# Kernel tuning notes

Measured on AMD Instinct MI355X. Metric: run time of the kernel, lower is better.

The kernel has to match this reference:

```python
import jax, jax.numpy as jnp
import numpy as np

BETA = 0.4
EPS = 0.05
NUM_CLASSES = 5


def _model_single(xi, W1, b1, W2, b2):
    # xi: [C, L] single sample -> logits [num_classes]
    h = jnp.tanh(xi.reshape(-1) @ W1 + b1)
    return h @ W2 + b2


def setup_inputs() -> dict:
    key = jax.random.key(0)
    k1, k2, k3, k4 = jax.random.split(key, 4)
    B, C, L, H = 8192, 1, 2048, 1024
    x = jax.random.normal(k1, (B, C, L), dtype=jnp.float32)
    y = jax.random.randint(k2, (B,), 0, NUM_CLASSES)
    W1 = jax.random.normal(k3, (C * L, H), dtype=jnp.float32) * (1.0 / np.sqrt(C * L).astype(np.float32))
    b1 = jnp.zeros((H,), dtype=jnp.float32)
    W2 = jax.random.normal(k4, (H, NUM_CLASSES), dtype=jnp.float32) * (1.0 / np.sqrt(H).astype(np.float32))
    b2 = jnp.zeros((NUM_CLASSES,), dtype=jnp.float32)
    return {"x": x, "y": y, "W1": W1, "b1": b1, "W2": W2, "b2": b2}


def reference(x, y, W1, b1, W2, b2):
    B = x.shape[0]
    # batched model forward (same math the torch loop calls per-sample)
    logits = jnp.tanh(x.reshape(B, -1) @ W1 + b1) @ W2 + b2  # [B, num_classes]

    y_onehot = jax.nn.one_hot(y, NUM_CLASSES, dtype=logits.dtype)
    mse_loss = jnp.mean((logits - y_onehot) ** 2)

    idx = jnp.arange(B)
    z_y = logits[idx, y]  # [B]
    margins = jnp.maximum(1.0 - z_y[:, None] + logits, 0.0)
    margins = margins.at[idx, y].set(0.0)
    margin_loss = margins.sum() / B

    # per-sample L1 norm of d z_y / d x_i: one batched vmap(grad) instead of a python loop
    def z_of_x(xi, yi):
        return _model_single(xi, W1, b1, W2, b2)[yi]

    grads = jax.vmap(jax.grad(z_of_x), in_axes=(0, 0))(x, y)  # [B, C, L]
    w_l1 = jnp.sum(jnp.abs(grads), axis=(1, 2))  # [B]

    R = w_l1 * EPS / (jnp.abs(z_y) + 1e-8)
    nsr_loss = BETA * jnp.mean(jnp.log1p(R))

    correct_mask = jnp.mean((jnp.argmax(logits, axis=1) == y).astype(logits.dtype))
    total_loss = mse_loss + (margin_loss + nsr_loss) * correct_mask
    return total_loss
```

## Files before the change

kernel.cpp:

```cpp
#include <hip/hip_runtime.h>
#include <hip/hip_bf16.h>

typedef unsigned short ushort_t;
typedef unsigned char uchar_t;
typedef __attribute__((ext_vector_type(8))) short short8;
typedef __attribute__((ext_vector_type(8))) unsigned short u16x8;
typedef __attribute__((ext_vector_type(4))) float f32x4;
typedef __attribute__((ext_vector_type(4))) int i32x4;

#define BETA 0.4f
#define EPS_C 0.05f
#define NB 8192
#define NH 1024
#define NL 2048
#define NC 5
#define VS_I8 800.0f
#define WS_I8 1200.0f

static __device__ __forceinline__ float b2f(unsigned short u) {
    union { unsigned int i; float f; } x; x.i = ((unsigned int)u) << 16; return x.f;
}
static __device__ __forceinline__ unsigned short f2b(float f) {
    union { float f; unsigned int i; } x; x.f = f;
    unsigned int i = x.i;
    unsigned int r = (i + 0x7FFFu + ((i >> 16) & 1u)) >> 16;
    return (unsigned short)r;
}
static __device__ __forceinline__ char f2i8(float f, float s) {
    float q = rintf(f * s);
    q = fminf(127.f, fmaxf(-127.f, q));
    return (char)(int)q;
}

static __device__ __forceinline__ void gload16(const ushort_t* g, ushort_t* l) {
    __builtin_amdgcn_global_load_lds((const __attribute__((address_space(1))) void*)g,
                                     (__attribute__((address_space(3))) void*)l, 16, 0, 0);
}
static __device__ __forceinline__ void gload16b(const uchar_t* g, uchar_t* l) {
    __builtin_amdgcn_global_load_lds((const __attribute__((address_space(1))) void*)g,
                                     (__attribute__((address_space(3))) void*)l, 16, 0, 0);
}

#define CFENCE() asm volatile("" ::: "memory")
#define MFMA16(d, a, b) __builtin_amdgcn_mfma_f32_16x16x32_bf16(a, b, d, 0, 0, 0)
#define MFMAI8(d, a, b) __builtin_amdgcn_mfma_i32_16x16x64_i8(a, b, d, 0, 0, 0)

__global__ __launch_bounds__(256) void cvt_kernel(const float* __restrict__ in,
                                                  ushort_t* __restrict__ out, long n) {
    long i = ((long)blockIdx.x * 256 + threadIdx.x) * 8;
    if (i >= n) return;
    const float4 a = *(const float4*)(in + i);
    const float4 b = *(const float4*)(in + i + 4);
    u16x8 o;
    o[0] = f2b(a.x); o[1] = f2b(a.y); o[2] = f2b(a.z); o[3] = f2b(a.w);
    o[4] = f2b(b.x); o[5] = f2b(b.y); o[6] = f2b(b.z); o[7] = f2b(b.w);
    *(u16x8*)(out + i) = o;
}

__global__ __launch_bounds__(256) void trans_kernel(const float* __restrict__ W1,
                                                    ushort_t* __restrict__ W1Tb,
                                                    char* __restrict__ W1i8) {
    __shared__ float tile[32][33];
    const int tx = threadIdx.x & 31, ty = threadIdx.x >> 5;
    const int k0 = blockIdx.x * 32, n0 = blockIdx.y * 32;
#pragma unroll
    for (int i = 0; i < 4; ++i) {
        const float v = W1[(size_t)(k0 + ty + i * 8) * NH + n0 + tx];
        tile[ty + i * 8][tx] = v;
        W1i8[(size_t)(k0 + ty + i * 8) * NH + n0 + tx] = f2i8(v, WS_I8);
    }
    __syncthreads();
#pragma unroll
    for (int i = 0; i < 4; ++i)
        W1Tb[(size_t)(n0 + ty + i * 8) * NL + k0 + tx] = f2b(tile[tx][ty + i * 8]);
}

__global__ __launch_bounds__(256, 2) void g128_1(const ushort_t* __restrict__ A,
                                                 const ushort_t* __restrict__ Bt,
                                                 const float* __restrict__ b1,
                                                 ushort_t* __restrict__ hout) {
    constexpr int K  = 2048;
    constexpr int NT = K / 64;

    __shared__ ushort_t As[2][8192];
    __shared__ ushort_t Bs[2][8192];

    const int tid = threadIdx.x;
    const int wv = tid >> 6, lane = tid & 63;
    const int wm = (wv >> 1) & 1, wn = wv & 1;
    const int fr = lane & 15, fg = lane >> 4;

    const int xcd = blockIdx.x & 7, loc = blockIdx.x >> 3;
    const int bm0 = (xcd * 8 + (loc >> 3)) * 128;
    const int bn0 = (loc & 7) * 128;

    const int srow = lane >> 3;
    const int scol = ((lane & 7) ^ srow) << 3;

#define STA(BUF, KT) {                                                      \
    _Pragma("unroll") for (int c_ = 0; c_ < 4; ++c_) {                      \
        const int row_ = c_ * 32 + wv * 8 + srow;                           \
        gload16(A + (size_t)(bm0 + row_) * K + (KT) * 64 + scol,            \
                &As[BUF][c_ * 2048 + wv * 512]);                            \
    } }
#define STB(BUF, KT) {                                                      \
    _Pragma("unroll") for (int c_ = 0; c_ < 4; ++c_) {                      \
        const int row_ = c_ * 32 + wv * 8 + srow;                           \
        gload16(Bt + (size_t)(bn0 + row_) * K + (KT) * 64 + scol,           \
                &Bs[BUF][c_ * 2048 + wv * 512]);                            \
    } }

    auto ldA = [&](int buf, int mf, int ks) -> short8 {
        const int row = wm * 64 + mf * 16 + fr;
        const int slot = ((ks << 2) + fg) ^ (row & 7);
        return *(const short8*)&As[buf][row * 64 + slot * 8];
    };
    auto ldB = [&](int buf, int nf, int ks) -> short8 {
        const int row = wn * 64 + nf * 16 + fr;
        const int slot = ((ks << 2) + fg) ^ (row & 7);
        return *(const short8*)&Bs[buf][row * 64 + slot * 8];
    };

    f32x4 acc[4][4] = {};

    STA(0, 0) STB(0, 0)
    asm volatile("s_waitcnt vmcnt(0)" ::: "memory");
    CFENCE(); __builtin_amdgcn_s_barrier(); CFENCE();

#define TILE(BUF, TT) {                                                     \
    const int t_ = (TT);                                                    \
    short8 af[4][2], bf[4][2];                                              \
    _Pragma("unroll") for (int n_ = 0; n_ < 4; ++n_) {                      \
        bf[n_][0] = ldB(BUF, n_, 0); bf[n_][1] = ldB(BUF, n_, 1);           \
    }                                                                       \
    _Pragma("unroll") for (int m_ = 0; m_ < 4; ++m_) {                      \
        af[m_][0] = ldA(BUF, m_, 0); af[m_][1] = ldA(BUF, m_, 1);           \
    }                                                                       \
    if (t_ + 1 < NT) { STA(BUF ^ 1, t_ + 1) STB(BUF ^ 1, t_ + 1) }          \
    CFENCE(); __builtin_amdgcn_s_barrier(); CFENCE();                       \
    __builtin_amdgcn_s_setprio(1);                                          \
    _Pragma("unroll") for (int m_ = 0; m_ < 4; ++m_)                        \
        _Pragma("unroll") for (int n_ = 0; n_ < 4; ++n_) {                  \
            acc[m_][n_] = MFMA16(acc[m_][n_], af[m_][0], bf[n_][0]);        \
            acc[m_][n_] = MFMA16(acc[m_][n_], af[m_][1], bf[n_][1]);        \
        }                                                                   \
    __builtin_amdgcn_s_setprio(0);                                          \
    asm volatile("s_waitcnt vmcnt(0)" ::: "memory");                        \
    CFENCE(); __builtin_amdgcn_s_barrier(); CFENCE();                       \
    }

#pragma unroll 1
    for (int t = 0; t < NT; t += 2) {
        TILE(0, t)
        TILE(1, t + 1)
    }
#undef TILE
#undef STA
#undef STB

#pragma unroll
    for (int m = 0; m < 4; ++m)
#pragma unroll
        for (int n = 0; n < 4; ++n) {
            const int col = bn0 + wn * 64 + n * 16 + fr;
            const float bb = b1[col];
            const size_t rbase = (size_t)(bm0 + wm * 64 + m * 16 + fg * 4) * NH + col;
#pragma unroll
            for (int r = 0; r < 4; ++r)
                hout[rbase + (size_t)r * NH] = f2b(tanhf(acc[m][n][r] + bb));
        }
}

__global__ __launch_bounds__(256, 4) void g2i8(const char* __restrict__ A,
                                               const char* __restrict__ Bt,
                                               float* __restrict__ partout) {
    constexpr int K  = 1024;
    constexpr int NT = K / 64;

    __shared__ uchar_t As[2][8192];
    __shared__ uchar_t Bs[2][8192];

    const int tid = threadIdx.x;
    const int wv = tid >> 6, lane = tid & 63;
    const int wm = (wv >> 1) & 1, wn = wv & 1;
    const int fr = lane & 15, fg = lane >> 4;

    const int xcd = blockIdx.x & 7, loc = blockIdx.x >> 3;
    const int bm0 = (xcd * 8 + (loc >> 4)) * 128;
    const int bnIdx = loc & 15;
    const int bn0 = bnIdx * 128;

    const int t8 = tid >> 3, t7 = tid & 7;

#define STAF(BUF, KT) {                                                     \
    _Pragma("unroll") for (int j_ = 0; j_ < 2; ++j_) {                      \
        const int r1_ = j_ * 32 + t8;                                       \
        const int sl_ = (t7 * 2) ^ ((r1_ & 7) << 1);                        \
        const int row_ = 2 * r1_ + (sl_ >> 3);                              \
        const int cb_ = (KT) * 64 + (sl_ & 7) * 8;                          \
        gload16b((const uchar_t*)A + (size_t)(bm0 + row_) * K + cb_,        \
                 &As[BUF][j_ * 4096 + wv * 1024]);                          \
    } }
#define STBF(BUF, KT) {                                                     \
    _Pragma("unroll") for (int j_ = 0; j_ < 2; ++j_) {                      \
        const int r1_ = j_ * 32 + t8;                                       \
        const int sl_ = (t7 * 2) ^ ((r1_ & 7) << 1);                        \
        const int row_ = 2 * r1_ + (sl_ >> 3);                              \
        const int cb_ = (KT) * 64 + (sl_ & 7) * 8;                          \
        gload16b((const uchar_t*)Bt + (size_t)(bn0 + row_) * K + cb_,       \
                 &Bs[BUF][j_ * 4096 + wv * 1024]);                          \
    } }

    auto ldA = [&](int buf, int mf) -> i32x4 {
        const int row = wm * 64 + mf * 16 + fr;
        const int r1 = row >> 1;
        const int phys = (((row & 1) << 3) | (fg << 1)) ^ ((r1 & 7) << 1);
        return *(const i32x4*)&As[buf][r1 * 128 + phys * 8];
    };
    auto ldB = [&](int buf, int nf) -> i32x4 {
        const int row = wn * 64 + nf * 16 + fr;
        const int r1 = row >> 1;
        const int phys = (((row & 1) << 3) | (fg << 1)) ^ ((r1 & 7) << 1);
        return *(const i32x4*)&Bs[buf][r1 * 128 + phys * 8];
    };

    i32x4 acc[4][4] = {};

    STAF(0, 0) STBF(0, 0)
    asm volatile("s_waitcnt vmcnt(0)" ::: "memory");
    CFENCE(); __builtin_amdgcn_s_barrier(); CFENCE();

#define TILEI(BUF, TT) {                                                    \
    const int t_ = (TT);                                                    \
    i32x4 af[4], bf[4];                                                     \
    _Pragma("unroll") for (int n_ = 0; n_ < 4; ++n_) bf[n_] = ldB(BUF, n_); \
    _Pragma("unroll") for (int m_ = 0; m_ < 4; ++m_) af[m_] = ldA(BUF, m_); \
    if (t_ + 1 < NT) { STAF(BUF ^ 1, t_ + 1) STBF(BUF ^ 1, t_ + 1) }        \
    CFENCE(); __builtin_amdgcn_s_barrier(); CFENCE();                       \
    __builtin_amdgcn_s_setprio(1);                                          \
    _Pragma("unroll") for (int m_ = 0; m_ < 4; ++m_)                        \
        _Pragma("unroll") for (int n_ = 0; n_ < 4; ++n_)                    \
            acc[m_][n_] = MFMAI8(acc[m_][n_], af[m_], bf[n_]);              \
    __builtin_amdgcn_s_setprio(0);                                          \
    asm volatile("s_waitcnt vmcnt(0)" ::: "memory");                        \
    CFENCE(); __builtin_amdgcn_s_barrier(); CFENCE();                       \
    }

#pragma unroll 1
    for (int t = 0; t < NT; t += 2) {
        TILEI(0, t)
        TILEI(1, t + 1)
    }
#undef TILEI
#undef STAF
#undef STBF

    __syncthreads();
    float* rsum = (float*)&As[0][0];
#pragma unroll
    for (int m = 0; m < 4; ++m)
#pragma unroll
        for (int r = 0; r < 4; ++r) {
            float s = 0.f;
#pragma unroll
            for (int n = 0; n < 4; ++n) s += fabsf((float)acc[m][n][r]);
            s += __shfl_xor(s, 1); s += __shfl_xor(s, 2);
            s += __shfl_xor(s, 4); s += __shfl_xor(s, 8);
            if (fr == 0) rsum[wn * 128 + wm * 64 + m * 16 + fg * 4 + r] = s;
        }
    __syncthreads();
    if (tid < 128)
        partout[(size_t)bnIdx * NB + bm0 + tid] = rsum[tid] + rsum[128 + tid];
}

__global__ __launch_bounds__(256) void rows_kernel(const ushort_t* __restrict__ hb,
                                                   const int* __restrict__ y,
                                                   const float* __restrict__ W2,
                                                   const float* __restrict__ b2,
                                                   char* __restrict__ vb,
                                                   float4* __restrict__ rowstats) {
    __shared__ float w2t[NC][NH];
    __shared__ float b2s[NC];
    const int tid = threadIdx.x;
    for (int i = tid; i < NH * NC; i += 256) w2t[i % NC][i / NC] = W2[i];
    if (tid < NC) b2s[tid] = b2[tid];
    __syncthreads();
    const int wid = tid >> 6, lane = tid & 63;
    const int row = blockIdx.x * 4 + wid;
    const ushort_t* hrow = hb + (size_t)row * NH;
    char* vrow = vb + (size_t)row * NH;
    const int yi = y[row];
    float d0 = 0, d1 = 0, d2 = 0, d3 = 0, d4 = 0;
#pragma unroll
    for (int it = 0; it < 2; ++it) {
        const int n0 = it * 512 + lane * 8;
        u16x8 hv = *(const u16x8*)(hrow + n0);
        float hh[8];
#pragma unroll
        for (int j = 0; j < 8; ++j) hh[j] = b2f(hv[j]);
#pragma unroll
        for (int c = 0; c < NC; ++c) {
            const float4 a = *(const float4*)&w2t[c][n0];
            const float4 b = *(const float4*)&w2t[c][n0 + 4];
            float d = hh[0] * a.x; d += hh[1] * a.y; d += hh[2] * a.z; d += hh[3] * a.w;
            d += hh[4] * b.x; d += hh[5] * b.y; d += hh[6] * b.z; d += hh[7] * b.w;
            if (c == 0) d0 += d; else if (c == 1) d1 += d; else if (c == 2) d2 += d;
            else if (c == 3) d3 += d; else d4 += d;
        }
        const float4 ya = *(const float4*)&w2t[yi][n0];
        const float4 yb = *(const float4*)&w2t[yi][n0 + 4];
        const float yw[8] = { ya.x, ya.y, ya.z, ya.w, yb.x, yb.y, yb.z, yb.w };
        union { char b[8]; long l; } ov;
#pragma unroll
        for (int j = 0; j < 8; ++j)
            ov.b[j] = f2i8((1.f - hh[j] * hh[j]) * yw[j], VS_I8);
        *(long*)(vrow + n0) = ov.l;
    }
#pragma unroll
    for (int off = 32; off; off >>= 1) {
        d0 += __shfl_xor(d0, off); d1 += __shfl_xor(d1, off); d2 += __shfl_xor(d2, off);
        d3 += __shfl_xor(d3, off); d4 += __shfl_xor(d4, off);
    }
    if (lane == 0) {
        float lg[NC] = { d0 + b2s[0], d1 + b2s[1], d2 + b2s[2], d3 + b2s[3], d4 + b2s[4] };
        float zy = lg[yi];
        float mse = 0.f, marg = 0.f;
        int amax = 0; float best = lg[0];
#pragma unroll
        for (int c = 0; c < NC; ++c) {
            float t = lg[c] - (c == yi ? 1.f : 0.f);
            mse += t * t;
            if (c != yi) marg += fmaxf(1.f - zy + lg[c], 0.f);
            if (lg[c] > best) { best = lg[c]; amax = c; }
        }
        rowstats[row] = make_float4(zy, mse, marg, (amax == yi) ? 1.f : 0.f);
    }
}

__global__ __launch_bounds__(256) void reduce_rows(const float4* __restrict__ rs,
                                                   const float* __restrict__ part,
                                                   int NT, float4* __restrict__ bsums) {
    const int tid = threadIdx.x;
    const int r = blockIdx.x * 256 + tid;
    float4 v = rs[r];
    float wl1 = 0.f;
    for (int t = 0; t < NT; ++t) wl1 += part[(size_t)t * NB + r];
    wl1 *= (1.0f / (VS_I8 * WS_I8));
    float R = wl1 * EPS_C / (fabsf(v.x) + 1e-8f);
    float4 s = make_float4(v.y, v.z, v.w, log1pf(R));
#pragma unroll
    for (int off = 32; off; off >>= 1) {
        s.x += __shfl_down(s.x, off); s.y += __shfl_down(s.y, off);
        s.z += __shfl_down(s.z, off); s.w += __shfl_down(s.w, off);
    }
    __shared__ float4 red[4];
    if ((tid & 63) == 0) red[tid >> 6] = s;
    __syncthreads();
    if (tid == 0) {
        float4 t = red[0];
        for (int i = 1; i < 4; ++i) { t.x += red[i].x; t.y += red[i].y; t.z += red[i].z; t.w += red[i].w; }
        bsums[blockIdx.x] = t;
    }
}

__global__ void final_combine(const float4* __restrict__ bsums, int nb, float* __restrict__ out) {
    const int l = threadIdx.x;
    float4 s = (l < nb) ? bsums[l] : make_float4(0.f, 0.f, 0.f, 0.f);
#pragma unroll
    for (int off = 32; off; off >>= 1) {
        s.x += __shfl_down(s.x, off); s.y += __shfl_down(s.y, off);
        s.z += __shfl_down(s.z, off); s.w += __shfl_down(s.w, off);
    }
    if (l == 0) {
        const float Bf = (float)NB;
        out[0] = s.x / (Bf * (float)NC) + (s.y / Bf + BETA * s.w / Bf) * (s.z / Bf);
    }
}

extern "C" void kernel_launch(void* const* d_in, const int* in_sizes, int n_in,
                              void* d_out, int out_size, void* d_ws, size_t ws_size,
                              hipStream_t stream) {
    const float* x  = (const float*)d_in[0];
    const int*   y  = (const int*)d_in[1];
    const float* W1 = (const float*)d_in[2];
    const float* b1 = (const float*)d_in[3];
    const float* W2 = (const float*)d_in[4];
    const float* b2 = (const float*)d_in[5];
    float* out = (float*)d_out;

    char* ws = (char*)d_ws;
    ushort_t* W1Tb = (ushort_t*)(ws);
    char*     W1i8 = (char*)(ws + (4ul << 20));
    ushort_t* xb   = (ushort_t*)(ws + (8ul << 20));
    ushort_t* hb   = (ushort_t*)(ws + (40ul << 20));
    char*     vi8  = (char*)(ws + (56ul << 20));
    float4*   rowstats = (float4*)(ws + (72ul << 20));
    float*    part = (float*)(ws + (72ul << 20) + (1ul << 20));
    float4*   bsums = (float4*)(ws + (74ul << 20));

    cvt_kernel<<<(NB * (long)NL) / (256 * 8), 256, 0, stream>>>(x, xb, (long)NB * NL);
    trans_kernel<<<dim3(NL / 32, NH / 32), 256, 0, stream>>>(W1, W1Tb, W1i8);

    g128_1<<<512, 256, 0, stream>>>(xb, W1Tb, b1, hb);

    rows_kernel<<<NB / 4, 256, 0, stream>>>(hb, y, W2, b2, vi8, rowstats);

    g2i8<<<1024, 256, 0, stream>>>(vi8, W1i8, part);

    reduce_rows<<<NB / 256, 256, 0, stream>>>(rowstats, part, NL / 128, bsums);
    final_combine<<<1, 64, 0, stream>>>(bsums, NB / 256, out);
}
```

Before: 106.7 us.

## Fuse fp32-to-bf16 conversion of x into first GEMM's A-tile loading

Drops the standalone cvt_kernel that wrote a bf16 copy of x, and has the first GEMM read fp32 x directly into registers. It converts the values with v_cvt_pk_bf16_f32 and writes them swizzled into LDS, double-buffered across tiles. This removes one kernel launch and a 64MB-read/32MB-write round trip through global memory. In exchange the GEMM reads twice as many bytes for A, uses more registers to hold the prefetched float4s, and adds an LDS write plus lgkmcnt wait before each barrier.

```diff
diff --git a/kernel.cpp b/kernel.cpp
--- a/kernel.cpp
+++ b/kernel.cpp
@@ -7,6 +7,7 @@
 typedef __attribute__((ext_vector_type(8))) unsigned short u16x8;
 typedef __attribute__((ext_vector_type(4))) float f32x4;
 typedef __attribute__((ext_vector_type(4))) int i32x4;
+typedef __attribute__((ext_vector_type(4))) unsigned int u32x4;
 
 #define BETA 0.4f
 #define EPS_C 0.05f
@@ -31,6 +32,11 @@
     q = fminf(127.f, fmaxf(-127.f, q));
     return (char)(int)q;
 }
+static __device__ __forceinline__ unsigned int cvtpk(float lo, float hi) {
+    unsigned int r;
+    asm("v_cvt_pk_bf16_f32 %0, %1, %2" : "=v"(r) : "v"(lo), "v"(hi));
+    return r;
+}
 
 static __device__ __forceinline__ void gload16(const ushort_t* g, ushort_t* l) {
     __builtin_amdgcn_global_load_lds((const __attribute__((address_space(1))) void*)g,
@@ -44,18 +50,6 @@
 #define CFENCE() asm volatile("" ::: "memory")
 #define MFMA16(d, a, b) __builtin_amdgcn_mfma_f32_16x16x32_bf16(a, b, d, 0, 0, 0)
 #define MFMAI8(d, a, b) __builtin_amdgcn_mfma_i32_16x16x64_i8(a, b, d, 0, 0, 0)
-
-__global__ __launch_bounds__(256) void cvt_kernel(const float* __restrict__ in,
-                                                  ushort_t* __restrict__ out, long n) {
-    long i = ((long)blockIdx.x * 256 + threadIdx.x) * 8;
-    if (i >= n) return;
-    const float4 a = *(const float4*)(in + i);
-    const float4 b = *(const float4*)(in + i + 4);
-    u16x8 o;
-    o[0] = f2b(a.x); o[1] = f2b(a.y); o[2] = f2b(a.z); o[3] = f2b(a.w);
-    o[4] = f2b(b.x); o[5] = f2b(b.y); o[6] = f2b(b.z); o[7] = f2b(b.w);
-    *(u16x8*)(out + i) = o;
-}
 
 __global__ __launch_bounds__(256) void trans_kernel(const float* __restrict__ W1,
                                                     ushort_t* __restrict__ W1Tb,
@@ -75,10 +69,10 @@
         W1Tb[(size_t)(n0 + ty + i * 8) * NL + k0 + tx] = f2b(tile[tx][ty + i * 8]);
 }
 
-__global__ __launch_bounds__(256, 2) void g128_1(const ushort_t* __restrict__ A,
-                                                 const ushort_t* __restrict__ Bt,
-                                                 const float* __restrict__ b1,
-                                                 ushort_t* __restrict__ hout) {
+__global__ __launch_bounds__(256, 2) void g128_1f(const float* __restrict__ X,
+                                                  const ushort_t* __restrict__ Bt,
+                                                  const float* __restrict__ b1,
+                                                  ushort_t* __restrict__ hout) {
     constexpr int K  = 2048;
     constexpr int NT = K / 64;
 
@@ -95,19 +89,30 @@
     const int bn0 = (loc & 7) * 128;
 
     const int srow = lane >> 3;
-    const int scol = ((lane & 7) ^ srow) << 3;
-
-#define STA(BUF, KT) {                                                      \
-    _Pragma("unroll") for (int c_ = 0; c_ < 4; ++c_) {                      \
-        const int row_ = c_ * 32 + wv * 8 + srow;                           \
-        gload16(A + (size_t)(bm0 + row_) * K + (KT) * 64 + scol,            \
-                &As[BUF][c_ * 2048 + wv * 512]);                            \
-    } }
+    const int scolb = ((lane & 7) ^ srow) << 3;
+    const int scolf = ((lane & 7) ^ srow) * 8;
+
 #define STB(BUF, KT) {                                                      \
     _Pragma("unroll") for (int c_ = 0; c_ < 4; ++c_) {                      \
         const int row_ = c_ * 32 + wv * 8 + srow;                           \
-        gload16(Bt + (size_t)(bn0 + row_) * K + (KT) * 64 + scol,           \
+        gload16(Bt + (size_t)(bn0 + row_) * K + (KT) * 64 + scolb,          \
                 &Bs[BUF][c_ * 2048 + wv * 512]);                            \
+    } }
+#define LDX(XA, KT) {                                                       \
+    _Pragma("unroll") for (int c_ = 0; c_ < 4; ++c_) {                      \
+        const int row_ = c_ * 32 + wv * 8 + srow;                           \
+        const float* p_ = X + (size_t)(bm0 + row_) * K + (KT) * 64 + scolf; \
+        XA[c_][0] = *(const float4*)p_;                                     \
+        XA[c_][1] = *(const float4*)(p_ + 4);                               \
+    } }
+#define WRX(BUF, XA) {                                                      \
+    _Pragma("unroll") for (int c_ = 0; c_ < 4; ++c_) {                      \
+        u32x4 w_;                                                           \
+        w_[0] = cvtpk(XA[c_][0].x, XA[c_][0].y);                            \
+        w_[1] = cvtpk(XA[c_][0].z, XA[c_][0].w);                            \
+        w_[2] = cvtpk(XA[c_][1].x, XA[c_][1].y);                            \
+        w_[3] = cvtpk(XA[c_][1].z, XA[c_][1].w);                            \
+        *(u32x4*)&As[BUF][c_ * 2048 + wv * 512 + lane * 8] = w_;            \
     } }
 
     auto ldA = [&](int buf, int mf, int ks) -> short8 {
@@ -122,13 +127,18 @@
     };
 
     f32x4 acc[4][4] = {};
-
-    STA(0, 0) STB(0, 0)
+    float4 xa[4][2];
+
+    LDX(xa, 0)
+    STB(0, 0)
     asm volatile("s_waitcnt vmcnt(0)" ::: "memory");
+    WRX(0, xa)
+    asm volatile("s_waitcnt lgkmcnt(0)" ::: "memory");
     CFENCE(); __builtin_amdgcn_s_barrier(); CFENCE();
 
 #define TILE(BUF, TT) {                                                     \
     const int t_ = (TT);                                                    \
+    const bool more = (t_ + 1 < NT);                                        \
     short8 af[4][2], bf[4][2];                                              \
     _Pragma("unroll") for (int n_ = 0; n_ < 4; ++n_) {                      \
         bf[n_][0] = ldB(BUF, n_, 0); bf[n_][1] = ldB(BUF, n_, 1);           \
@@ -136,7 +146,7 @@
     _Pragma("unroll") for (int m_ = 0; m_ < 4; ++m_) {                      \
         af[m_][0] = ldA(BUF, m_, 0); af[m_][1] = ldA(BUF, m_, 1);           \
     }                                                                       \
-    if (t_ + 1 < NT) { STA(BUF ^ 1, t_ + 1) STB(BUF ^ 1, t_ + 1) }          \
+    if (more) { LDX(xa, t_ + 1) STB(BUF ^ 1, t_ + 1) }                      \
     CFENCE(); __builtin_amdgcn_s_barrier(); CFENCE();                       \
     __builtin_amdgcn_s_setprio(1);                                          \
     _Pragma("unroll") for (int m_ = 0; m_ < 4; ++m_)                        \
@@ -146,6 +156,8 @@
         }                                                                   \
     __builtin_amdgcn_s_setprio(0);                                          \
     asm volatile("s_waitcnt vmcnt(0)" ::: "memory");                        \
+    if (more) { WRX(BUF ^ 1, xa) }                                          \
+    asm volatile("s_waitcnt lgkmcnt(0)" ::: "memory");                      \
     CFENCE(); __builtin_amdgcn_s_barrier(); CFENCE();                       \
     }
 
@@ -155,8 +167,9 @@
         TILE(1, t + 1)
     }
 #undef TILE
-#undef STA
 #undef STB
+#undef LDX
+#undef WRX
 
 #pragma unroll
     for (int m = 0; m < 4; ++m)
@@ -391,17 +404,15 @@
     char* ws = (char*)d_ws;
     ushort_t* W1Tb = (ushort_t*)(ws);
     char*     W1i8 = (char*)(ws + (4ul << 20));
-    ushort_t* xb   = (ushort_t*)(ws + (8ul << 20));
     ushort_t* hb   = (ushort_t*)(ws + (40ul << 20));
     char*     vi8  = (char*)(ws + (56ul << 20));
     float4*   rowstats = (float4*)(ws + (72ul << 20));
     float*    part = (float*)(ws + (72ul << 20) + (1ul << 20));
     float4*   bsums = (float4*)(ws + (74ul << 20));
 
-    cvt_kernel<<<(NB * (long)NL) / (256 * 8), 256, 0, stream>>>(x, xb, (long)NB * NL);
     trans_kernel<<<dim3(NL / 32, NH / 32), 256, 0, stream>>>(W1, W1Tb, W1i8);
 
-    g128_1<<<512, 256, 0, stream>>>(xb, W1Tb, b1, hb);
+    g128_1f<<<512, 256, 0, stream>>>(x, W1Tb, b1, hb);
 
     rows_kernel<<<NB / 4, 256, 0, stream>>>(hb, y, W2, b2, vi8, rowstats);
 
```

Measured after the change: 104.7 us. Within noise of the previous version (-1.9%).

## Quantize forward GEMM to int8 and share the int8 GEMM kernel via template

Applied to the files above, without the earlier changes.

The first GEMM (x @ W1) now runs on int8 MFMA instead of bf16. x is quantized with a fixed scale of 32 and W1^T with a scale of 1200, and the accumulator is rescaled in the tanh epilogue. This halves the bytes written by the conversion pass and read by the GEMM, and uses the faster int8 MFMA path. The cost is precision: x is normal-distributed and a fixed scale of 32 clips values beyond about 4 sigma, which adds quantization error to the hidden activations and therefore to the loss.

```diff
diff --git a/kernel.cpp b/kernel.cpp
--- a/kernel.cpp
+++ b/kernel.cpp
@@ -16,6 +16,8 @@
 #define NC 5
 #define VS_I8 800.0f
 #define WS_I8 1200.0f
+#define XS_I8 32.0f
+#define G1_INV (1.0f / (XS_I8 * WS_I8))
 
 static __device__ __forceinline__ float b2f(unsigned short u) {
     union { unsigned int i; float f; } x; x.i = ((unsigned int)u) << 16; return x.f;
@@ -32,33 +34,32 @@
     return (char)(int)q;
 }
 
-static __device__ __forceinline__ void gload16(const ushort_t* g, ushort_t* l) {
-    __builtin_amdgcn_global_load_lds((const __attribute__((address_space(1))) void*)g,
-                                     (__attribute__((address_space(3))) void*)l, 16, 0, 0);
-}
 static __device__ __forceinline__ void gload16b(const uchar_t* g, uchar_t* l) {
     __builtin_amdgcn_global_load_lds((const __attribute__((address_space(1))) void*)g,
                                      (__attribute__((address_space(3))) void*)l, 16, 0, 0);
 }
 
 #define CFENCE() asm volatile("" ::: "memory")
-#define MFMA16(d, a, b) __builtin_amdgcn_mfma_f32_16x16x32_bf16(a, b, d, 0, 0, 0)
 #define MFMAI8(d, a, b) __builtin_amdgcn_mfma_i32_16x16x64_i8(a, b, d, 0, 0, 0)
 
-__global__ __launch_bounds__(256) void cvt_kernel(const float* __restrict__ in,
-                                                  ushort_t* __restrict__ out, long n) {
-    long i = ((long)blockIdx.x * 256 + threadIdx.x) * 8;
+__global__ __launch_bounds__(256) void cvt8_kernel(const float* __restrict__ in,
+                                                   char* __restrict__ out, long n) {
+    long i = ((long)blockIdx.x * 256 + threadIdx.x) * 16;
     if (i >= n) return;
-    const float4 a = *(const float4*)(in + i);
-    const float4 b = *(const float4*)(in + i + 4);
-    u16x8 o;
-    o[0] = f2b(a.x); o[1] = f2b(a.y); o[2] = f2b(a.z); o[3] = f2b(a.w);
-    o[4] = f2b(b.x); o[5] = f2b(b.y); o[6] = f2b(b.z); o[7] = f2b(b.w);
-    *(u16x8*)(out + i) = o;
+    union { char b[16]; i32x4 v; } o;
+#pragma unroll
+    for (int q = 0; q < 4; ++q) {
+        const float4 a = *(const float4*)(in + i + q * 4);
+        o.b[q * 4 + 0] = f2i8(a.x, XS_I8);
+        o.b[q * 4 + 1] = f2i8(a.y, XS_I8);
+        o.b[q * 4 + 2] = f2i8(a.z, XS_I8);
+        o.b[q * 4 + 3] = f2i8(a.w, XS_I8);
+    }
+    *(i32x4*)(out + i) = o.v;
 }
 
 __global__ __launch_bounds__(256) void trans_kernel(const float* __restrict__ W1,
-                                                    ushort_t* __restrict__ W1Tb,
+                                                    char* __restrict__ W1Ti8,
                                                     char* __restrict__ W1i8) {
     __shared__ float tile[32][33];
     const int tx = threadIdx.x & 31, ty = threadIdx.x >> 5;
@@ -72,18 +73,20 @@
     __syncthreads();
 #pragma unroll
     for (int i = 0; i < 4; ++i)
-        W1Tb[(size_t)(n0 + ty + i * 8) * NL + k0 + tx] = f2b(tile[tx][ty + i * 8]);
-}
-
-__global__ __launch_bounds__(256, 2) void g128_1(const ushort_t* __restrict__ A,
-                                                 const ushort_t* __restrict__ Bt,
-                                                 const float* __restrict__ b1,
-                                                 ushort_t* __restrict__ hout) {
-    constexpr int K  = 2048;
+        W1Ti8[(size_t)(n0 + ty + i * 8) * NL + k0 + tx] = f2i8(tile[tx][ty + i * 8], WS_I8);
+}
+
+template <int EPI>
+__global__ __launch_bounds__(256, 4) void gi8(const char* __restrict__ A,
+                                              const char* __restrict__ Bt,
+                                              const float* __restrict__ b1,
+                                              ushort_t* __restrict__ hout,
+                                              float* __restrict__ partout) {
+    constexpr int K  = (EPI == 0) ? 2048 : 1024;
     constexpr int NT = K / 64;
 
-    __shared__ ushort_t As[2][8192];
-    __shared__ ushort_t Bs[2][8192];
+    __shared__ uchar_t As[2][8192];
+    __shared__ uchar_t Bs[2][8192];
 
     const int tid = threadIdx.x;
     const int wv = tid >> 6, lane = tid & 63;
@@ -91,103 +94,9 @@
     const int fr = lane & 15, fg = lane >> 4;
 
     const int xcd = blockIdx.x & 7, loc = blockIdx.x >> 3;
-    const int bm0 = (xcd * 8 + (loc >> 3)) * 128;
-    const int bn0 = (loc & 7) * 128;
-
-    const int srow = lane >> 3;
-    const int scol = ((lane & 7) ^ srow) << 3;
-
-#define STA(BUF, KT) {                                                      \
-    _Pragma("unroll") for (int c_ = 0; c_ < 4; ++c_) {                      \
-        const int row_ = c_ * 32 + wv * 8 + srow;                           \
-        gload16(A + (size_t)(bm0 + row_) * K + (KT) * 64 + scol,            \
-                &As[BUF][c_ * 2048 + wv * 512]);                            \
-    } }
-#define STB(BUF, KT) {                                                      \
-    _Pragma("unroll") for (int c_ = 0; c_ < 4; ++c_) {                      \
-        const int row_ = c_ * 32 + wv * 8 + srow;                           \
-        gload16(Bt + (size_t)(bn0 + row_) * K + (KT) * 64 + scol,           \
-                &Bs[BUF][c_ * 2048 + wv * 512]);                            \
-    } }
-
-    auto ldA = [&](int buf, int mf, int ks) -> short8 {
-        const int row = wm * 64 + mf * 16 + fr;
-        const int slot = ((ks << 2) + fg) ^ (row & 7);
-        return *(const short8*)&As[buf][row * 64 + slot * 8];
-    };
-    auto ldB = [&](int buf, int nf, int ks) -> short8 {
-        const int row = wn * 64 + nf * 16 + fr;
-        const int slot = ((ks << 2) + fg) ^ (row & 7);
-        return *(const short8*)&Bs[buf][row * 64 + slot * 8];
-    };
-
-    f32x4 acc[4][4] = {};
-
-    STA(0, 0) STB(0, 0)
-    asm volatile("s_waitcnt vmcnt(0)" ::: "memory");
-    CFENCE(); __builtin_amdgcn_s_barrier(); CFENCE();
-
-#define TILE(BUF, TT) {                                                     \
-    const int t_ = (TT);                                                    \
-    short8 af[4][2], bf[4][2];                                              \
-    _Pragma("unroll") for (int n_ = 0; n_ < 4; ++n_) {                      \
-        bf[n_][0] = ldB(BUF, n_, 0); bf[n_][1] = ldB(BUF, n_, 1);           \
-    }                                                                       \
-    _Pragma("unroll") for (int m_ = 0; m_ < 4; ++m_) {                      \
-        af[m_][0] = ldA(BUF, m_, 0); af[m_][1] = ldA(BUF, m_, 1);           \
-    }                                                                       \
-    if (t_ + 1 < NT) { STA(BUF ^ 1, t_ + 1) STB(BUF ^ 1, t_ + 1) }          \
-    CFENCE(); __builtin_amdgcn_s_barrier(); CFENCE();                       \
-    __builtin_amdgcn_s_setprio(1);                                          \
-    _Pragma("unroll") for (int m_ = 0; m_ < 4; ++m_)                        \
-        _Pragma("unroll") for (int n_ = 0; n_ < 4; ++n_) {                  \
-            acc[m_][n_] = MFMA16(acc[m_][n_], af[m_][0], bf[n_][0]);        \
-            acc[m_][n_] = MFMA16(acc[m_][n_], af[m_][1], bf[n_][1]);        \
-        }                                                                   \
-    __builtin_amdgcn_s_setprio(0);                                          \
-    asm volatile("s_waitcnt vmcnt(0)" ::: "memory");                        \
-    CFENCE(); __builtin_amdgcn_s_barrier(); CFENCE();                       \
-    }
-
-#pragma unroll 1
-    for (int t = 0; t < NT; t += 2) {
-        TILE(0, t)
-        TILE(1, t + 1)
-    }
-#undef TILE
-#undef STA
-#undef STB
-
-#pragma unroll
-    for (int m = 0; m < 4; ++m)
-#pragma unroll
-        for (int n = 0; n < 4; ++n) {
-            const int col = bn0 + wn * 64 + n * 16 + fr;
-            const float bb = b1[col];
-            const size_t rbase = (size_t)(bm0 + wm * 64 + m * 16 + fg * 4) * NH + col;
-#pragma unroll
-            for (int r = 0; r < 4; ++r)
-                hout[rbase + (size_t)r * NH] = f2b(tanhf(acc[m][n][r] + bb));
-        }
-}
-
-__global__ __launch_bounds__(256, 4) void g2i8(const char* __restrict__ A,
-                                               const char* __restrict__ Bt,
-                                               float* __restrict__ partout) {
-    constexpr int K  = 1024;
-    constexpr int NT = K / 64;
-
-    __shared__ uchar_t As[2][8192];
-    __shared__ uchar_t Bs[2][8192];
-
-    const int tid = threadIdx.x;
-    const int wv = tid >> 6, lane = tid & 63;
-    const int wm = (wv >> 1) & 1, wn = wv & 1;
-    const int fr = lane & 15, fg = lane >> 4;
-
-    const int xcd = blockIdx.x & 7, loc = blockIdx.x >> 3;
-    const int bm0 = (xcd * 8 + (loc >> 4)) * 128;
-    const int bnIdx = loc & 15;
+    const int bm0 = (EPI == 0) ? (xcd * 8 + (loc >> 3)) * 128
+                               : (xcd * 8 + (loc >> 4)) * 128;
+    const int bnIdx = (EPI == 0) ? (loc & 7) : (loc & 15);
     const int bn0 = bnIdx * 128;
 
     const int t8 = tid >> 3, t7 = tid & 7;
@@ -255,22 +164,37 @@
 #undef STAF
 #undef STBF
 
-    __syncthreads();
-    float* rsum = (float*)&As[0][0];
-#pragma unroll
-    for (int m = 0; m < 4; ++m)
-#pragma unroll
-        for (int r = 0; r < 4; ++r) {
-            float s = 0.f;
-#pragma unroll
-            for (int n = 0; n < 4; ++n) s += fabsf((float)acc[m][n][r]);
-            s += __shfl_xor(s, 1); s += __shfl_xor(s, 2);
-            s += __shfl_xor(s, 4); s += __shfl_xor(s, 8);
-            if (fr == 0) rsum[wn * 128 + wm * 64 + m * 16 + fg * 4 + r] = s;
-        }
-    __syncthreads();
-    if (tid < 128)
-        partout[(size_t)bnIdx * NB + bm0 + tid] = rsum[tid] + rsum[128 + tid];
+    if constexpr (EPI == 0) {
+#pragma unroll
+        for (int m = 0; m < 4; ++m)
+#pragma unroll
+            for (int n = 0; n < 4; ++n) {
+                const int col = bn0 + wn * 64 + n * 16 + fr;
+                const float bb = b1[col];
+                const size_t rbase = (size_t)(bm0 + wm * 64 + m * 16 + fg * 4) * NH + col;
+#pragma unroll
+                for (int r = 0; r < 4; ++r)
+                    hout[rbase + (size_t)r * NH] =
+                        f2b(tanhf((float)acc[m][n][r] * G1_INV + bb));
+            }
+    } else {
+        __syncthreads();
+        float* rsum = (float*)&As[0][0];
+#pragma unroll
+        for (int m = 0; m < 4; ++m)
+#pragma unroll
+            for (int r = 0; r < 4; ++r) {
+                float s = 0.f;
+#pragma unroll
+                for (int n = 0; n < 4; ++n) s += fabsf((float)acc[m][n][r]);
+                s += __shfl_xor(s, 1); s += __shfl_xor(s, 2);
+                s += __shfl_xor(s, 4); s += __shfl_xor(s, 8);
+                if (fr == 0) rsum[wn * 128 + wm * 64 + m * 16 + fg * 4 + r] = s;
+            }
+        __syncthreads();
+        if (tid < 128)
+            partout[(size_t)bnIdx * NB + bm0 + tid] = rsum[tid] + rsum[128 + tid];
+    }
 }
 
 __global__ __launch_bounds__(256) void rows_kernel(const ushort_t* __restrict__ hb,
@@ -389,23 +313,23 @@
     float* out = (float*)d_out;
 
     char* ws = (char*)d_ws;
-    ushort_t* W1Tb = (ushort_t*)(ws);
-    char*     W1i8 = (char*)(ws + (4ul << 20));
-    ushort_t* xb   = (ushort_t*)(ws + (8ul << 20));
-    ushort_t* hb   = (ushort_t*)(ws + (40ul << 20));
-    char*     vi8  = (char*)(ws + (56ul << 20));
+    char*     W1Ti8 = (char*)(ws);
+    char*     W1i8  = (char*)(ws + (4ul << 20));
+    char*     xi8   = (char*)(ws + (8ul << 20));
+    ushort_t* hb    = (ushort_t*)(ws + (40ul << 20));
+    char*     vi8   = (char*)(ws + (56ul << 20));
     float4*   rowstats = (float4*)(ws + (72ul << 20));
     float*    part = (float*)(ws + (72ul << 20) + (1ul << 20));
     float4*   bsums = (float4*)(ws + (74ul << 20));
 
-    cvt_kernel<<<(NB * (long)NL) / (256 * 8), 256, 0, stream>>>(x, xb, (long)NB * NL);
-    trans_kernel<<<dim3(NL / 32, NH / 32), 256, 0, stream>>>(W1, W1Tb, W1i8);
-
-    g128_1<<<512, 256, 0, stream>>>(xb, W1Tb, b1, hb);
+    cvt8_kernel<<<(NB * (long)NL) / (256 * 16), 256, 0, stream>>>(x, xi8, (long)NB * NL);
+    trans_kernel<<<dim3(NL / 32, NH / 32), 256, 0, stream>>>(W1, W1Ti8, W1i8);
+
+    gi8<0><<<512, 256, 0, stream>>>(xi8, W1Ti8, b1, hb, nullptr);
 
     rows_kernel<<<NB / 4, 256, 0, stream>>>(hb, y, W2, b2, vi8, rowstats);
 
-    g2i8<<<1024, 256, 0, stream>>>(vi8, W1i8, part);
+    gi8<1><<<1024, 256, 0, stream>>>(vi8, W1i8, nullptr, nullptr, part);
 
     reduce_rows<<<NB / 256, 256, 0, stream>>>(rowstats, part, NL / 128, bsums);
     final_combine<<<1, 64, 0, stream>>>(bsums, NB / 256, out);
```

Measured after the change: 92.87 us. -13.0%, faster.
